# Kernel tuning notes

Measured on AMD Instinct MI355X. Metric: run time of the kernel, lower is better.

## Reference

```python
import jax, jax.numpy as jnp
import numpy as np

D = 1024          # dim_in == dim_out
H = 16            # num_heads
G = 4             # num_kv_groups
HD = D // H       # head_dim = 64
GS = H // G       # group_size = 4
S = 2048          # context_length / seq_len
B = 2
EPS = 1e-05


def setup_inputs() -> dict:
    key = jax.random.key(0)
    ks = jax.random.split(key, 12)
    sd = 0.02
    return {
        "x":  jax.random.normal(ks[0], (B, S, D), jnp.float32),
        # torch.nn.Linear weights are stored [out_features, in_features]
        "wq": jax.random.normal(ks[1], (D, D), jnp.float32) * sd,
        "wk": jax.random.normal(ks[2], (G * HD, D), jnp.float32) * sd,
        "wv": jax.random.normal(ks[3], (G * HD, D), jnp.float32) * sd,
        "wo": jax.random.normal(ks[4], (D, D), jnp.float32) * sd,
        "w1": jax.random.normal(ks[5], (4 * D, D), jnp.float32) * sd,
        "w2": jax.random.normal(ks[6], (D, 4 * D), jnp.float32) * sd,
        "g1": jnp.ones((D,), jnp.float32),
        "b1": jnp.zeros((D,), jnp.float32),
        "g2": jnp.ones((D,), jnp.float32),
        "b2": jnp.zeros((D,), jnp.float32),
    }


def _layernorm(x, gamma, beta):
    mean = jnp.mean(x, axis=-1, keepdims=True)
    var = jnp.var(x, axis=-1, keepdims=True)  # unbiased=False
    return (x - mean) * jax.lax.rsqrt(var + EPS) * gamma + beta


def _gelu_tanh(x):
    c = jnp.sqrt(jnp.asarray(2.0 / jnp.pi, x.dtype))
    return 0.5 * x * (1.0 + jnp.tanh(c * (x + 0.044715 * x ** 3)))


def _gqa(x, wq, wk, wv, wo):
    b, s, _ = x.shape
    q = (x @ wq.T).reshape(b, s, H, HD).transpose(0, 2, 1, 3)   # [B,H,S,hd]
    k = (x @ wk.T).reshape(b, s, G, HD).transpose(0, 2, 1, 3)   # [B,G,S,hd]
    v = (x @ wv.T).reshape(b, s, G, HD).transpose(0, 2, 1, 3)
    k = jnp.repeat(k, GS, axis=1)                               # [B,H,S,hd]
    v = jnp.repeat(v, GS, axis=1)
    scores = jnp.einsum('bhqd,bhkd->bhqk', q, k)                # [B,H,S,S]
    causal = jnp.tril(jnp.ones((s, s), bool))
    scores = jnp.where(causal, scores, -jnp.inf)
    attn = jax.nn.softmax(scores / jnp.sqrt(jnp.asarray(HD, scores.dtype)), axis=-1)
    ctx = jnp.einsum('bhqk,bhkd->bhqd', attn, v)                # [B,H,S,hd]
    ctx = ctx.transpose(0, 2, 1, 3).reshape(b, s, D)
    return ctx @ wo.T


def reference(x, wq, wk, wv, wo, w1, w2, g1, b1, g2, b2):
    h = x + _gqa(_layernorm(x, g1, b1), wq, wk, wv, wo)
    ff = _layernorm(h, g2, b2) @ w1.T
    ff = _gelu_tanh(ff) @ w2.T
    return h + ff
```

## Files before the change

kernel.cpp:

```cpp
#include <hip/hip_runtime.h>
#include <stdint.h>

typedef __bf16 bf16_t;
typedef bf16_t bf16x8 __attribute__((ext_vector_type(8)));
typedef bf16_t bf16x4 __attribute__((ext_vector_type(4)));
typedef float f32x4 __attribute__((ext_vector_type(4)));

#define DEVFN static __device__ __forceinline__

DEVFN void gload_lds16(const void* g, void* l) {
  __builtin_amdgcn_global_load_lds((const __attribute__((address_space(1))) void*)g,
                                   (__attribute__((address_space(3))) void*)l, 16, 0, 0);
}

DEVFN float gelu_f(float x) {
  float u = 0.7978845608028654f * (x + 0.044715f * x * x * x);
  float e = __expf(2.0f * u);
  float t = 1.0f - 2.0f / (e + 1.0f);
  return 0.5f * x * (1.0f + t);
}

template <int CTRL>
DEVFN float dpp_rot(float x) {
  int i = __builtin_bit_cast(int, x);
  int r = __builtin_amdgcn_update_dpp(i, i, CTRL, 0xF, 0xF, false);
  return __builtin_bit_cast(float, r);
}
DEVFN float dpp_sum16(float x) {
  x += dpp_rot<0x121>(x);
  x += dpp_rot<0x122>(x);
  x += dpp_rot<0x124>(x);
  x += dpp_rot<0x128>(x);
  return x;
}

__global__ void cvt_kernel(const float* __restrict__ s, bf16_t* __restrict__ d, int n4) {
  int i = blockIdx.x * blockDim.x + threadIdx.x;
  int stride = gridDim.x * blockDim.x;
  for (; i < n4; i += stride) {
    float4 v = ((const float4*)s)[i];
    bf16x4 o;
    o[0] = (bf16_t)v.x; o[1] = (bf16_t)v.y; o[2] = (bf16_t)v.z; o[3] = (bf16_t)v.w;
    ((bf16x4*)d)[i] = o;
  }
}

__global__ void cvt4_kernel(const float* __restrict__ wq, const float* __restrict__ wk,
                            const float* __restrict__ wv, const float* __restrict__ wo,
                            bf16_t* __restrict__ qkv_dst, bf16_t* __restrict__ wo_dst) {
  int i = blockIdx.x * blockDim.x + threadIdx.x;
  int stride = gridDim.x * blockDim.x;
  for (; i < 655360; i += stride) {
    const float* s;
    bf16_t* d;
    int j;
    if (i < 262144) { s = wq; d = qkv_dst; j = i; }
    else if (i < 327680) { s = wk; d = qkv_dst + 1048576; j = i - 262144; }
    else if (i < 393216) { s = wv; d = qkv_dst + 1310720; j = i - 327680; }
    else { s = wo; d = wo_dst; j = i - 393216; }
    float4 v = ((const float4*)s)[j];
    bf16x4 o;
    o[0] = (bf16_t)v.x; o[1] = (bf16_t)v.y; o[2] = (bf16_t)v.z; o[3] = (bf16_t)v.w;
    ((bf16x4*)d)[j] = o;
  }
}

__global__ __launch_bounds__(256) void ln_kernel(const float* __restrict__ in,
                                                 const float* __restrict__ gamma,
                                                 const float* __restrict__ beta,
                                                 bf16_t* __restrict__ out) {
  const int row = blockIdx.x;
  const int tid = threadIdx.x;
  const float4 v = ((const float4*)(in + (size_t)row * 1024))[tid];
  float s = v.x + v.y + v.z + v.w;
  float q = v.x * v.x + v.y * v.y + v.z * v.z + v.w * v.w;
#pragma unroll
  for (int off = 1; off < 64; off <<= 1) {
    s += __shfl_xor(s, off);
    q += __shfl_xor(q, off);
  }
  __shared__ float ss[4], qs[4];
  if ((tid & 63) == 0) { ss[tid >> 6] = s; qs[tid >> 6] = q; }
  __syncthreads();
  s = ss[0] + ss[1] + ss[2] + ss[3];
  q = qs[0] + qs[1] + qs[2] + qs[3];
  const float mean = s * (1.0f / 1024.0f);
  const float var = q * (1.0f / 1024.0f) - mean * mean;
  const float rstd = rsqrtf(var + 1e-5f);
  const float4 g4 = ((const float4*)gamma)[tid];
  const float4 b4 = ((const float4*)beta)[tid];
  bf16x4 o;
  o[0] = (bf16_t)((v.x - mean) * rstd * g4.x + b4.x);
  o[1] = (bf16_t)((v.y - mean) * rstd * g4.y + b4.y);
  o[2] = (bf16_t)((v.z - mean) * rstd * g4.z + b4.z);
  o[3] = (bf16_t)((v.w - mean) * rstd * g4.w + b4.w);
  *(bf16x4*)(out + (size_t)row * 1024 + tid * 4) = o;
}

template <int EPI, int BM>
__global__ __launch_bounds__(256, (BM == 64 ? 3 : 2))
void gemm_bt(const bf16_t* __restrict__ A, const bf16_t* __restrict__ W,
             bf16_t* outb, float* outf, const float* resid, int M, int N, int K) {
  constexpr int MI = BM / 32;
  constexpr int WRS = BM / 2;
  __shared__ __align__(16) bf16_t As[2][2][BM * 32];
  __shared__ __align__(16) bf16_t Bs[2][2][128 * 32];
  const int tid = threadIdx.x;
  const int lane = tid & 63;
  const int wid = tid >> 6;
  const int l15 = lane & 15;
  const int l4 = lane >> 4;

  const int nwg = gridDim.x * gridDim.y;
  const int bid = blockIdx.y * gridDim.x + blockIdx.x;
  const int cpx = nwg >> 3;
  const int swz = (bid & 7) * cpx + (bid >> 3);
  const int m0 = (swz / gridDim.x) * BM;
  const int n0 = (swz % gridDim.x) * 128;

  const int wr = wid >> 1;
  const int wc = wid & 1;

  const int sr = lane >> 2;
  const int sk = (lane & 3) * 8;
  const bf16_t* aBase;
  if constexpr (BM == 128) aBase = A + (size_t)(m0 + wid * 32 + sr) * K + sk;
  else                     aBase = A + (size_t)(m0 + wid * 16 + sr) * K + sk;
  const bf16_t* bBase = W + (size_t)(n0 + wid * 32 + sr) * K + sk;
  const size_t rowOff16 = (size_t)16 * K;

  f32x4 acc[MI][4] = {};
  const int NT = K / 64;

  auto stage = [&](int buf, int t) {
    const int kt = t * 64;
#pragma unroll
    for (int kk = 0; kk < 2; ++kk) {
      const int ko = kt + kk * 32;
      if constexpr (BM == 128) {
        gload_lds16(aBase + ko, &As[buf][kk][wid * 1024]);
        gload_lds16(aBase + ko + rowOff16, &As[buf][kk][wid * 1024 + 512]);
      } else {
        gload_lds16(aBase + ko, &As[buf][kk][wid * 512]);
      }
      gload_lds16(bBase + ko, &Bs[buf][kk][wid * 1024]);
      gload_lds16(bBase + ko + rowOff16, &Bs[buf][kk][wid * 1024 + 512]);
    }
  };

  stage(0, 0);
  for (int t = 0; t < NT; ++t) {
    __syncthreads();
    if (t + 1 < NT) stage((t + 1) & 1, t + 1);
    const int buf = t & 1;
#pragma unroll
    for (int kk = 0; kk < 2; ++kk) {
      bf16x8 af[MI], bfr[4];
#pragma unroll
      for (int i = 0; i < MI; ++i)
        af[i] = *(const bf16x8*)&As[buf][kk][(wr * WRS + i * 16 + l15) * 32 + l4 * 8];
#pragma unroll
      for (int j = 0; j < 4; ++j)
        bfr[j] = *(const bf16x8*)&Bs[buf][kk][(wc * 64 + j * 16 + l15) * 32 + l4 * 8];
#pragma unroll
      for (int i = 0; i < MI; ++i)
#pragma unroll
        for (int j = 0; j < 4; ++j)
          acc[i][j] = __builtin_amdgcn_mfma_f32_16x16x32_bf16(af[i], bfr[j], acc[i][j], 0, 0, 0);
    }
  }

  const int col0 = n0 + wc * 64 + l15;
  const int row0 = m0 + wr * WRS + l4 * 4;
#pragma unroll
  for (int i = 0; i < MI; ++i) {
#pragma unroll
    for (int r = 0; r < 4; ++r) {
      const size_t row = (size_t)(row0 + i * 16 + r);
#pragma unroll
      for (int j = 0; j < 4; ++j) {
        const size_t idx = row * N + col0 + j * 16;
        const float v = acc[i][j][r];
        if constexpr (EPI == 0) {
          outb[idx] = (bf16_t)v;
        } else if constexpr (EPI == 1) {
          outb[idx] = (bf16_t)gelu_f(v);
        } else {
          outf[idx] = resid[idx] + v;
        }
      }
    }
  }
}

static __device__ const int kQbTab[40] = {0,1,2,3,4,4,5,5,6,6,7,7,8,8,8,9,9,9,10,10,10,
                                          11,11,11,12,12,12,12,13,13,13,13,14,14,14,14,15,15,15,15};
static __device__ const int kCTab[40]  = {0,0,0,0,0,1,0,1,0,1,0,1,0,1,2,0,1,2,0,1,2,
                                          0,1,2,0,1,2,3,0,1,2,3,0,1,2,3,0,1,2,3};
static __device__ const int kPrefix16[16] = {0,1,2,3,4,6,8,10,12,15,18,21,24,28,32,36};

__global__ __launch_bounds__(256, 3) void attn_kernel(const bf16_t* __restrict__ qkv,
                                                      bf16_t* __restrict__ pO,
                                                      float* __restrict__ pML) {
  __shared__ __align__(16) bf16_t Ks[2][64 * 68];
  __shared__ __align__(16) bf16_t Vt[2][64 * 68];
  __shared__ __align__(16) bf16_t Ps[4][32 * 68];
  const int tid = threadIdx.x, lane = tid & 63, wid = tid >> 6;
  const int l15 = lane & 15, l4 = lane >> 4;
  const int bx = blockIdx.x;
  const int qb = kQbTab[bx] * 128;
  const int kv_lo = kCTab[bx] * 512;
  const int kv_hi = min(qb + 128, kv_lo + 512);
  const int h = blockIdx.y, b = blockIdx.z;
  const int g = h >> 2;
  const int slot = (b * 16 + h) * 40 + bx;
  const size_t RS = 1536;
  const bf16_t* qbase = qkv + (size_t)b * 2048 * RS + h * 64;
  const bf16_t* kbase = qkv + (size_t)b * 2048 * RS + 1024 + g * 64;
  const bf16_t* vbase = kbase + 256;
  const float C2S = 0.125f * 1.44269504088896340736f;

  bf16x8 qf[2][2];
#pragma unroll
  for (int rf = 0; rf < 2; ++rf)
#pragma unroll
    for (int kc = 0; kc < 2; ++kc) {
      bf16x8 raw = *(const bf16x8*)(qbase + (size_t)(qb + wid * 32 + rf * 16 + l15) * RS +
                                    kc * 32 + l4 * 8);
#pragma unroll
      for (int e = 0; e < 8; ++e) qf[rf][kc][e] = (bf16_t)((float)raw[e] * C2S);
    }

  f32x4 po[2][4] = {};
  float l_i[2][4] = {};

  const int sKrow = tid >> 2, sKc = (tid & 3) * 16;
  const int sVkey = tid & 63, sVd = (tid >> 6) * 16;
  const bf16_t* kRowPtr = kbase + (size_t)sKrow * RS + sKc;
  const bf16_t* vRowPtr = vbase + (size_t)sVkey * RS + sVd;

  uint4 k0 = *(const uint4*)(kRowPtr + (size_t)kv_lo * RS);
  uint4 k1 = *(const uint4*)(kRowPtr + (size_t)kv_lo * RS + 8);
  bf16x8 v0 = *(const bf16x8*)(vRowPtr + (size_t)kv_lo * RS);
  bf16x8 v1 = *(const bf16x8*)(vRowPtr + (size_t)kv_lo * RS + 8);
  *(uint4*)&Ks[0][sKrow * 68 + sKc] = k0;
  *(uint4*)&Ks[0][sKrow * 68 + sKc + 8] = k1;
#pragma unroll
  for (int i = 0; i < 8; ++i) {
    Vt[0][(sVd + i) * 68 + sVkey] = v0[i];
    Vt[0][(sVd + 8 + i) * 68 + sVkey] = v1[i];
  }

  const int fb0 = qb + wid * 32;
  int cur = 0;
  for (int kv0 = kv_lo; kv0 < kv_hi; kv0 += 64) {
    __syncthreads();
    const bool more = (kv0 + 64) < kv_hi;
    if (more) {
      const bf16_t* kp = kRowPtr + (size_t)(kv0 + 64) * RS;
      const bf16_t* vp = vRowPtr + (size_t)(kv0 + 64) * RS;
      k0 = *(const uint4*)kp;
      k1 = *(const uint4*)(kp + 8);
      v0 = *(const bf16x8*)vp;
      v1 = *(const bf16x8*)(vp + 8);
    }

    f32x4 sAcc[2][4] = {};
#pragma unroll
    for (int jt = 0; jt < 4; ++jt) {
#pragma unroll
      for (int kc = 0; kc < 2; ++kc) {
        bf16x8 kf = *(const bf16x8*)&Ks[cur][(jt * 16 + l15) * 68 + kc * 32 + l4 * 8];
        sAcc[0][jt] = __builtin_amdgcn_mfma_f32_16x16x32_bf16(qf[0][kc], kf, sAcc[0][jt], 0, 0, 0);
        sAcc[1][jt] = __builtin_amdgcn_mfma_f32_16x16x32_bf16(qf[1][kc], kf, sAcc[1][jt], 0, 0, 0);
      }
    }

#pragma unroll
    for (int rf = 0; rf < 2; ++rf) {
      const int fb = fb0 + rf * 16;
      if (kv0 > fb + 15) continue;
      bf16_t* psb = &Ps[wid][(rf * 16 + l4 * 4) * 68 + l15];
      float rsum[4] = {0.f, 0.f, 0.f, 0.f};
      const bool diag = (kv0 + 63 > fb);
#pragma unroll
      for (int jt = 0; jt < 4; ++jt)
#pragma unroll
        for (int r = 0; r < 4; ++r) {
          float sv = sAcc[rf][jt][r];
          if (diag) {
            const int key = kv0 + jt * 16 + l15;
            sv = (key <= fb + l4 * 4 + r) ? sv : -3.0e38f;
          }
          const float e = exp2f(sv);
          rsum[r] += e;
          psb[r * 68 + jt * 16] = (bf16_t)e;
        }
#pragma unroll
      for (int r = 0; r < 4; ++r) l_i[rf][r] += dpp_sum16(rsum[r]);
    }

    if (kv0 <= fb0 + 31) {
      const bool do0 = (kv0 <= fb0 + 15);
#pragma unroll
      for (int kc = 0; kc < 2; ++kc) {
        bf16x8 pa1 = *(const bf16x8*)&Ps[wid][(16 + l15) * 68 + kc * 32 + l4 * 8];
        bf16x8 pa0;
        if (do0) pa0 = *(const bf16x8*)&Ps[wid][l15 * 68 + kc * 32 + l4 * 8];
#pragma unroll
        for (int jd = 0; jd < 4; ++jd) {
          bf16x8 vf = *(const bf16x8*)&Vt[cur][(jd * 16 + l15) * 68 + kc * 32 + l4 * 8];
          if (do0) po[0][jd] = __builtin_amdgcn_mfma_f32_16x16x32_bf16(pa0, vf, po[0][jd], 0, 0, 0);
          po[1][jd] = __builtin_amdgcn_mfma_f32_16x16x32_bf16(pa1, vf, po[1][jd], 0, 0, 0);
        }
      }
    }

    if (more) {
      *(uint4*)&Ks[cur ^ 1][sKrow * 68 + sKc] = k0;
      *(uint4*)&Ks[cur ^ 1][sKrow * 68 + sKc + 8] = k1;
#pragma unroll
      for (int i = 0; i < 8; ++i) {
        Vt[cur ^ 1][(sVd + i) * 68 + sVkey] = v0[i];
        Vt[cur ^ 1][(sVd + 8 + i) * 68 + sVkey] = v1[i];
      }
    }
    cur ^= 1;
  }

#pragma unroll
  for (int rf = 0; rf < 2; ++rf) {
#pragma unroll
    for (int r = 0; r < 4; ++r) {
      const int lrow = wid * 32 + rf * 16 + l4 * 4 + r;
      if (l15 == 0) {
        pML[((size_t)slot * 128 + lrow) * 2] = 0.0f;
        pML[((size_t)slot * 128 + lrow) * 2 + 1] = l_i[rf][r];
      }
#pragma unroll
      for (int jd = 0; jd < 4; ++jd)
        pO[((size_t)slot * 128 + lrow) * 64 + jd * 16 + l15] = (bf16_t)po[rf][jd][r];
    }
  }
}

__global__ __launch_bounds__(256) void attn_combine(const bf16_t* __restrict__ pO,
                                                    const float* __restrict__ pML,
                                                    bf16_t* __restrict__ ctx) {
  const int i = blockIdx.x, h = blockIdx.y, b = blockIdx.z;
  const int C = (i >> 2) + 1;
  const int base = (b * 16 + h) * 40 + kPrefix16[i];
  const int row = threadIdx.x >> 1;
  const int half = (threadIdx.x & 1) * 32;
  float m = -3.0e38f;
  for (int c = 0; c < C; ++c)
    m = fmaxf(m, pML[((size_t)(base + c) * 128 + row) * 2]);
  float L = 0.0f, acc[32];
#pragma unroll
  for (int e = 0; e < 32; ++e) acc[e] = 0.0f;
  for (int c = 0; c < C; ++c) {
    const float mc = pML[((size_t)(base + c) * 128 + row) * 2];
    const float lc = pML[((size_t)(base + c) * 128 + row) * 2 + 1];
    const float w = exp2f(mc - m);
    L += w * lc;
    const bf16_t* op = pO + ((size_t)(base + c) * 128 + row) * 64 + half;
#pragma unroll
    for (int j = 0; j < 4; ++j) {
      bf16x8 v = *(const bf16x8*)(op + j * 8);
#pragma unroll
      for (int e = 0; e < 8; ++e) acc[j * 8 + e] += w * (float)v[e];
    }
  }
  const float inv = 1.0f / L;
  bf16_t* outp = ctx + ((size_t)b * 2048 + i * 128 + row) * 1024 + h * 64 + half;
#pragma unroll
  for (int j = 0; j < 4; ++j) {
    bf16x8 o;
#pragma unroll
    for (int e = 0; e < 8; ++e) o[e] = (bf16_t)(acc[j * 8 + e] * inv);
    *(bf16x8*)(outp + j * 8) = o;
  }
}

extern "C" void kernel_launch(void* const* d_in, const int* in_sizes, int n_in,
                              void* d_out, int out_size, void* d_ws, size_t ws_size,
                              hipStream_t stream) {
  const float* x = (const float*)d_in[0];
  const float* wq = (const float*)d_in[1];
  const float* wk = (const float*)d_in[2];
  const float* wv = (const float*)d_in[3];
  const float* wo = (const float*)d_in[4];
  const float* w1 = (const float*)d_in[5];
  const float* w2 = (const float*)d_in[6];
  const float* g1 = (const float*)d_in[7];
  const float* b1 = (const float*)d_in[8];
  const float* g2 = (const float*)d_in[9];
  const float* b2 = (const float*)d_in[10];
  float* out = (float*)d_out;

  char* ws = (char*)d_ws;
  bf16_t* qkv = (bf16_t*)(ws + 0);
  bf16_t* ctx = (bf16_t*)(ws + 12582912);
  bf16_t* wo_b = (bf16_t*)(ws + 20971520);
  bf16_t* wqkv_b = (bf16_t*)(ws + 23068672);
  bf16_t* h1 = (bf16_t*)(ws + 26214400);
  bf16_t* pO = (bf16_t*)(ws + 23068672);
  float* pML = (float*)(ws + 45088768);
  bf16_t* w1_b = (bf16_t*)(ws + 0);
  bf16_t* w2_b = (bf16_t*)(ws + 8388608);
  bf16_t* h2 = (bf16_t*)(ws + 16777216);
  bf16_t* ff = (bf16_t*)(ws + 25165824);

  auto cvt = [&](const float* s, bf16_t* d, int n) {
    int n4 = n / 4;
    int grid = (n4 + 255) / 256;
    if (grid > 2048) grid = 2048;
    cvt_kernel<<<grid, 256, 0, stream>>>(s, d, n4);
  };
  cvt4_kernel<<<2048, 256, 0, stream>>>(wq, wk, wv, wo, wqkv_b, wo_b);

  ln_kernel<<<4096, 256, 0, stream>>>(x, g1, b1, h1);
  gemm_bt<0, 64><<<dim3(12, 64), 256, 0, stream>>>(h1, wqkv_b, qkv, nullptr, nullptr, 4096, 1536, 1024);
  attn_kernel<<<dim3(40, 16, 2), 256, 0, stream>>>(qkv, pO, pML);
  cvt(w1, w1_b, 4194304);
  attn_combine<<<dim3(16, 16, 2), 256, 0, stream>>>(pO, pML, ctx);
  gemm_bt<2, 64><<<dim3(8, 64), 256, 0, stream>>>(ctx, wo_b, nullptr, out, x, 4096, 1024, 1024);
  cvt(w2, w2_b, 4194304);
  ln_kernel<<<4096, 256, 0, stream>>>(out, g2, b2, h2);
  gemm_bt<1, 128><<<dim3(32, 32), 256, 0, stream>>>(h2, w1_b, ff, nullptr, nullptr, 4096, 4096, 1024);
  gemm_bt<2, 64><<<dim3(8, 64), 256, 0, stream>>>(ff, w2_b, nullptr, out, out, 4096, 1024, 4096);
}
```

Measured before the change: 253.0 us.

## Split-K the FF2 GEMM into two halves and shrink FF1 tile

The final FF2 GEMM (K=4096) is split along K into two z-slices. Slice 0 writes residual+partial to the fp32 output and slice 1 writes its partial in bf16 to a scratch buffer, which a new elementwise kernel adds into the output. This doubles the workgroup count for the long-K GEMM to improve CU occupancy. Separately, the FF1 GEMM switches from 128-row to 64-row tiles with a larger grid. The costs are an extra launch, extra memory traffic, and bf16 rounding of the second partial sum.

Result: slower. 271.1 us (+7.2%).

```diff
diff --git a/kernel.cpp b/kernel.cpp
--- a/kernel.cpp
+++ b/kernel.cpp
@@ -65,6 +65,18 @@
   }
 }
 
+__global__ __launch_bounds__(256) void ff2add_kernel(float* __restrict__ out,
+                                                     const bf16_t* __restrict__ p1) {
+  const int i = blockIdx.x * 256 + threadIdx.x;
+  bf16x8 v = ((const bf16x8*)p1)[i];
+  float4 a = ((const float4*)out)[2 * i];
+  float4 b = ((const float4*)out)[2 * i + 1];
+  a.x += (float)v[0]; a.y += (float)v[1]; a.z += (float)v[2]; a.w += (float)v[3];
+  b.x += (float)v[4]; b.y += (float)v[5]; b.z += (float)v[6]; b.w += (float)v[7];
+  ((float4*)out)[2 * i] = a;
+  ((float4*)out)[2 * i + 1] = b;
+}
+
 __global__ __launch_bounds__(256) void ln_kernel(const float* __restrict__ in,
                                                  const float* __restrict__ gamma,
                                                  const float* __restrict__ beta,
@@ -100,7 +112,7 @@
 template <int EPI, int BM>
 __global__ __launch_bounds__(256, (BM == 64 ? 3 : 2))
 void gemm_bt(const bf16_t* __restrict__ A, const bf16_t* __restrict__ W,
-             bf16_t* outb, float* outf, const float* resid, int M, int N, int K) {
+             bf16_t* outb, float* outf, const float* resid, int M, int N, int K, int KL) {
   constexpr int MI = BM / 32;
   constexpr int WRS = BM / 2;
   __shared__ __align__(16) bf16_t As[2][2][BM * 32];
@@ -117,6 +129,7 @@
   const int swz = (bid & 7) * cpx + (bid >> 3);
   const int m0 = (swz / gridDim.x) * BM;
   const int n0 = (swz % gridDim.x) * 128;
+  const int kOff = blockIdx.z * KL;
 
   const int wr = wid >> 1;
   const int wc = wid & 1;
@@ -124,13 +137,13 @@
   const int sr = lane >> 2;
   const int sk = (lane & 3) * 8;
   const bf16_t* aBase;
-  if constexpr (BM == 128) aBase = A + (size_t)(m0 + wid * 32 + sr) * K + sk;
-  else                     aBase = A + (size_t)(m0 + wid * 16 + sr) * K + sk;
-  const bf16_t* bBase = W + (size_t)(n0 + wid * 32 + sr) * K + sk;
+  if constexpr (BM == 128) aBase = A + (size_t)(m0 + wid * 32 + sr) * K + sk + kOff;
+  else                     aBase = A + (size_t)(m0 + wid * 16 + sr) * K + sk + kOff;
+  const bf16_t* bBase = W + (size_t)(n0 + wid * 32 + sr) * K + sk + kOff;
   const size_t rowOff16 = (size_t)16 * K;
 
   f32x4 acc[MI][4] = {};
-  const int NT = K / 64;
+  const int NT = KL / 64;
 
   auto stage = [&](int buf, int t) {
     const int kt = t * 64;
@@ -185,8 +198,11 @@
           outb[idx] = (bf16_t)v;
         } else if constexpr (EPI == 1) {
           outb[idx] = (bf16_t)gelu_f(v);
+        } else if constexpr (EPI == 2) {
+          outf[idx] = resid[idx] + v;
         } else {
-          outf[idx] = resid[idx] + v;
+          if (blockIdx.z == 0) outf[idx] = resid[idx] + v;
+          else                 outb[idx] = (bf16_t)v;
         }
       }
     }
@@ -410,6 +426,7 @@
   bf16_t* w2_b = (bf16_t*)(ws + 8388608);
   bf16_t* h2 = (bf16_t*)(ws + 16777216);
   bf16_t* ff = (bf16_t*)(ws + 25165824);
+  bf16_t* p1 = (bf16_t*)(ws + 16777216);
 
   auto cvt = [&](const float* s, bf16_t* d, int n) {
     int n4 = n / 4;
@@ -420,13 +437,18 @@
   cvt4_kernel<<<2048, 256, 0, stream>>>(wq, wk, wv, wo, wqkv_b, wo_b);
 
   ln_kernel<<<4096, 256, 0, stream>>>(x, g1, b1, h1);
-  gemm_bt<0, 64><<<dim3(12, 64), 256, 0, stream>>>(h1, wqkv_b, qkv, nullptr, nullptr, 4096, 1536, 1024);
+  gemm_bt<0, 64><<<dim3(12, 64), 256, 0, stream>>>(h1, wqkv_b, qkv, nullptr, nullptr,
+                                                   4096, 1536, 1024, 1024);
   attn_kernel<<<dim3(40, 16, 2), 256, 0, stream>>>(qkv, pO, pML);
   cvt(w1, w1_b, 4194304);
   attn_combine<<<dim3(16, 16, 2), 256, 0, stream>>>(pO, pML, ctx);
-  gemm_bt<2, 64><<<dim3(8, 64), 256, 0, stream>>>(ctx, wo_b, nullptr, out, x, 4096, 1024, 1024);
+  gemm_bt<2, 64><<<dim3(8, 64), 256, 0, stream>>>(ctx, wo_b, nullptr, out, x,
+                                                  4096, 1024, 1024, 1024);
   cvt(w2, w2_b, 4194304);
   ln_kernel<<<4096, 256, 0, stream>>>(out, g2, b2, h2);
-  gemm_bt<1, 128><<<dim3(32, 32), 256, 0, stream>>>(h2, w1_b, ff, nullptr, nullptr, 4096, 4096, 1024);
-  gemm_bt<2, 64><<<dim3(8, 64), 256, 0, stream>>>(ff, w2_b, nullptr, out, out, 4096, 1024, 4096);
-}
+  gemm_bt<1, 64><<<dim3(32, 64), 256, 0, stream>>>(h2, w1_b, ff, nullptr, nullptr,
+                                                   4096, 4096, 1024, 1024);
+  gemm_bt<3, 64><<<dim3(8, 64, 2), 256, 0, stream>>>(ff, w2_b, p1, out, out,
+                                                     4096, 1024, 4096, 2048);
+  ff2add_kernel<<<2048, 256, 0, stream>>>(out, p1);
+}
```
